# Kernel tuning notes

Measured on AMD Instinct MI355X. Metric: run time of the kernel, lower is better.

## Reference

```python
import jax, jax.numpy as jnp
import numpy as np

D_HEAD = 64
MASK_FILL = -1000000.0


def setup_inputs() -> dict:
    key = jax.random.key(0)
    ks = jax.random.split(key, 5)
    batch, seq, d_model, n_heads, d_head = 4, 2048, 1024, 16, D_HEAD
    # xavier_uniform bound for [d_model, n_heads, d_head]: treated as fan_in=d_model, fan_out=n_heads*d_head
    bound_qkv = float(np.sqrt(6.0 / (d_model + n_heads * d_head)))
    bound_out = float(np.sqrt(6.0 / (d_head + n_heads * d_model)))
    return {
        "resid": jax.random.normal(ks[0], (batch, seq, d_model), dtype=jnp.float32),
        "W_Q": jax.random.uniform(ks[1], (d_model, n_heads, d_head), jnp.float32, -bound_qkv, bound_qkv),
        "W_K": jax.random.uniform(ks[2], (d_model, n_heads, d_head), jnp.float32, -bound_qkv, bound_qkv),
        "W_V": jax.random.uniform(ks[3], (d_model, n_heads, d_head), jnp.float32, -bound_qkv, bound_qkv),
        "W_out": jax.random.uniform(ks[4], (d_head, n_heads, d_model), jnp.float32, -bound_out, bound_out),
        "b_out": jnp.zeros((d_model,), dtype=jnp.float32),
    }


def reference(resid, W_Q, W_K, W_V, W_out, b_out):
    # resid: [b, s, d]; W_Q/K/V: [d, h, dh]; W_out: [dh, h, d]
    seq = resid.shape[1]
    d_head = W_Q.shape[-1]
    q = jnp.einsum('bsd,dhk->bshk', resid, W_Q)
    k = jnp.einsum('bsd,dhk->bshk', resid, W_K)
    v = jnp.einsum('bsd,dhk->bshk', resid, W_V)
    scores = jnp.einsum('bqhk,bkhd->bhqd', q, k.astype(q.dtype)) if False else jnp.einsum('bqhc,bshc->bhqs', q, k)
    scores = scores / jnp.sqrt(jnp.asarray(d_head, dtype=scores.dtype))
    causal_mask = jnp.triu(jnp.ones((seq, seq), dtype=bool), k=1)
    scores = jnp.where(causal_mask, MASK_FILL, scores)
    probs = jax.nn.softmax(scores, axis=-1)  # [b, h, q, s]
    z = jnp.einsum('bhqs,bshc->bqhc', probs, v)
    out = jnp.einsum('bqhc,chd->bqd', z, W_out) + b_out
    return out
```

## Files before the change

kernel.cpp:

```cpp
#include <hip/hip_runtime.h>
#include <hip/hip_bf16.h>


typedef short s16x8 __attribute__((ext_vector_type(8)));
typedef short s16x4 __attribute__((ext_vector_type(4)));
typedef float f32x4 __attribute__((ext_vector_type(4)));

#define MFMA_BF16(A, B, C) __builtin_amdgcn_mfma_f32_16x16x32_bf16((A), (B), (C), 0, 0, 0)

__device__ __forceinline__ short f2bf(float f) {
    __bf16 h = (__bf16)f;
    return __builtin_bit_cast(short, h);
}

__device__ __forceinline__ void gld16(const unsigned short* g, unsigned short* l) {
    __builtin_amdgcn_global_load_lds(
        (const __attribute__((address_space(1))) unsigned int*)g,
        (__attribute__((address_space(3))) unsigned int*)l, 16, 0, 0);
}

__global__ __launch_bounds__(256) void cast_f32_to_bf16(const float* __restrict__ x,
                                                        unsigned short* __restrict__ y,
                                                        int n4) {
    const int i = blockIdx.x * 256 + threadIdx.x;
    if (i >= n4) return;
    const float4 v = ((const float4*)x)[i];
    s16x4 o;
    o[0] = f2bf(v.x); o[1] = f2bf(v.y); o[2] = f2bf(v.z); o[3] = f2bf(v.w);
    *(s16x4*)(y + (size_t)i * 4) = o;
}

__global__ __launch_bounds__(256) void transpose_w_to_bf16(const float* __restrict__ W,
                                                           unsigned short* __restrict__ Wt) {
    __shared__ unsigned short tile[64][66];
    const int n0 = blockIdx.x * 64, k0 = blockIdx.y * 64;
    const int tx = threadIdx.x & 63, ty = threadIdx.x >> 6;
    #pragma unroll
    for (int i = ty; i < 64; i += 4)
        tile[i][tx] = (unsigned short)f2bf(W[(size_t)(k0 + i) * 1024 + n0 + tx]);
    __syncthreads();
    #pragma unroll
    for (int i = ty; i < 64; i += 4)
        Wt[(size_t)(n0 + i) * 1024 + k0 + tx] = tile[tx][i];
}

__global__ __launch_bounds__(256) void transpose_wout_to_bf16(const float* __restrict__ Wout,
                                                              unsigned short* __restrict__ W2t) {
    __shared__ unsigned short tile[64][66];
    const int d0 = blockIdx.x * 64;
    const int h  = blockIdx.y;
    const int tx = threadIdx.x & 63, ty = threadIdx.x >> 6;
    #pragma unroll
    for (int c = ty; c < 64; c += 4)
        tile[c][tx] = (unsigned short)f2bf(Wout[(size_t)(c * 16 + h) * 1024 + d0 + tx]);
    __syncthreads();
    #pragma unroll
    for (int i = ty; i < 64; i += 4)
        W2t[(size_t)(d0 + i) * 1024 + h * 64 + tx] = tile[tx][i];
}

template <int MODE>
__global__ __launch_bounds__(256, 2) void gemm_bt(
    const unsigned short* __restrict__ A,
    const unsigned short* __restrict__ Bt,
    float* __restrict__ Cf, const float* __restrict__ bias,
    unsigned short* __restrict__ Qb, unsigned short* __restrict__ Kb,
    unsigned short* __restrict__ Vt,
    int M, int N, int K)
{
    __shared__ __align__(16) unsigned short As[128 * 32];
    __shared__ __align__(16) unsigned short Bs[128 * 32];
    const int tid  = threadIdx.x;
    const int lane = tid & 63;
    const int w    = tid >> 6;
    const int wm   = w & 1, wn = w >> 1;
    const int quad = lane >> 4, fl = lane & 15;
    const int m0 = blockIdx.y * 128, n0 = blockIdx.x * 128;
    const int lrow = tid >> 2;
    const int lcol = (tid & 3) * 8;

    const unsigned short* Ap = A  + (size_t)(m0 + lrow) * K + lcol;
    const unsigned short* Bp = Bt + (size_t)(n0 + lrow) * K + lcol;

    f32x4 acc[4][4];
    #pragma unroll
    for (int i = 0; i < 4; ++i)
        #pragma unroll
        for (int j = 0; j < 4; ++j)
            acc[i][j] = (f32x4){0.f, 0.f, 0.f, 0.f};

    for (int kt = 0; kt < K; kt += 32) {
        __syncthreads();
        gld16(Ap + kt,                 As + tid * 8);
        gld16(Ap + (size_t)64 * K + kt, As + 2048 + tid * 8);
        gld16(Bp + kt,                 Bs + tid * 8);
        gld16(Bp + (size_t)64 * K + kt, Bs + 2048 + tid * 8);
        __syncthreads();
        s16x8 af[4], bf[4];
        #pragma unroll
        for (int mi = 0; mi < 4; ++mi)
            af[mi] = *(const s16x8*)(As + (wm * 64 + mi * 16 + fl) * 32 + quad * 8);
        #pragma unroll
        for (int ni = 0; ni < 4; ++ni)
            bf[ni] = *(const s16x8*)(Bs + (wn * 64 + ni * 16 + fl) * 32 + quad * 8);
        #pragma unroll
        for (int mi = 0; mi < 4; ++mi)
            #pragma unroll
            for (int ni = 0; ni < 4; ++ni)
                acc[mi][ni] = MFMA_BF16(af[mi], bf[ni], acc[mi][ni]);
    }

    if (MODE == 0) {
        #pragma unroll
        for (int ni = 0; ni < 4; ++ni) {
            const int col = n0 + wn * 64 + ni * 16 + fl;
            const float bv = bias[col];
            #pragma unroll
            for (int mi = 0; mi < 4; ++mi) {
                const int row = m0 + wm * 64 + mi * 16 + quad * 4;
                #pragma unroll
                for (int r = 0; r < 4; ++r)
                    Cf[(size_t)(row + r) * N + col] = acc[mi][ni][r] + bv;
            }
        }
    } else {
        #pragma unroll
        for (int ni = 0; ni < 4; ++ni) {
            const int colg = n0 + wn * 64 + ni * 16 + fl;
            #pragma unroll
            for (int mi = 0; mi < 4; ++mi) {
                const int token = m0 + wm * 64 + mi * 16 + quad * 4;
                if (n0 < 1024) {
                    #pragma unroll
                    for (int r = 0; r < 4; ++r)
                        Qb[(size_t)(token + r) * 1024 + colg] = (unsigned short)f2bf(acc[mi][ni][r]);
                } else if (n0 < 2048) {
                    #pragma unroll
                    for (int r = 0; r < 4; ++r)
                        Kb[(size_t)(token + r) * 1024 + (colg - 1024)] = (unsigned short)f2bf(acc[mi][ni][r]);
                } else {
                    const int cc = colg - 2048;
                    const int hh = cc >> 6, cl = cc & 63;
                    const int bb = token >> 11, ss = token & 2047;
                    s16x4 pv;
                    pv[0] = f2bf(acc[mi][ni][0]); pv[1] = f2bf(acc[mi][ni][1]);
                    pv[2] = f2bf(acc[mi][ni][2]); pv[3] = f2bf(acc[mi][ni][3]);
                    *(s16x4*)(Vt + (size_t)((bb * 16 + hh) * 64 + cl) * 2048 + ss) = pv;
                }
            }
        }
    }
}

__global__ __launch_bounds__(256, 3) void attn_causal(
    const unsigned short* __restrict__ Qb,
    const unsigned short* __restrict__ Kb,
    const unsigned short* __restrict__ Vt,
    unsigned short* __restrict__ Zb)
{
    __shared__ __align__(16) unsigned short KV[17920];
    __shared__ __align__(16) unsigned short Pb[4][32 * 40];
    const int tid = threadIdx.x, lane = tid & 63, w = tid >> 6;
    const int quad = lane >> 4, fl = lane & 15;
    const int lid = blockIdx.x;
    const int qb = 15 - (lid >> 6);
    const int bh = lid & 63, b = bh >> 4, h = bh & 15;
    const int q0 = qb * 128 + w * 32;

    const unsigned short* Kbase = Kb + (size_t)b * 2048 * 1024 + h * 64;
    const unsigned short* Vbase = Vt + (size_t)bh * 64 * 2048;
    unsigned short* PbW = Pb[w];
    const unsigned short* Vs = KV + 9216;

    s16x8 qfr[2][2];
    #pragma unroll
    for (int g = 0; g < 2; ++g) {
        const unsigned short* Qrow = Qb + (size_t)(b * 2048 + q0 + g * 16 + fl) * 1024 + h * 64;
        qfr[g][0] = *(const s16x8*)(Qrow + quad * 8);
        qfr[g][1] = *(const s16x8*)(Qrow + 32 + quad * 8);
    }

    const unsigned short* gsp[9];
    int smul[9];
    unsigned ldsb[9];
    #pragma unroll
    for (int i = 0; i < 9; ++i) {
        const int W = w + 4 * i;
        if (W < 35) {
            const int c = W * 64 + lane;
            if (c < 1152) {
                const int r = c / 9, cl0 = c % 9;
                const int cl = (cl0 == 8) ? 0 : cl0;
                gsp[i] = Kbase + r * 1024 + cl * 8;  smul[i] = 1024;
            } else {
                const int cc = c - 1152;
                const int r = cc / 17, cl0 = cc % 17;
                const int cl = (cl0 == 16) ? 0 : cl0;
                gsp[i] = Vbase + r * 2048 + cl * 8;  smul[i] = 1;
            }
            ldsb[i] = (unsigned)c * 8u;
        }
    }

    f32x4 zt[2][4];
    #pragma unroll
    for (int g = 0; g < 2; ++g)
        #pragma unroll
        for (int mf = 0; mf < 4; ++mf) zt[g][mf] = (f32x4){0.f, 0.f, 0.f, 0.f};
    float ls[2] = {0.f, 0.f};
    const float SC = 0.18033688011112042f;
    const float M  = 32.0f;
    const int ntiles = qb + 1;

    for (int kt = 0; kt < ntiles; ++kt) {
        const int s0 = kt << 7;
        const bool diag = (kt == qb);
        __syncthreads();
        #pragma unroll
        for (int i = 0; i < 9; ++i)
            if (w + 4 * i < 35)
                gld16(gsp[i] + s0 * smul[i], KV + ldsb[i]);
        __syncthreads();

        #pragma unroll
        for (int c4 = 0; c4 < 4; ++c4) {
            if (diag && c4 > w) break;
            #pragma unroll
            for (int e = 0; e < 2; ++e) {
                const int f = 2 * c4 + e;
                const unsigned short* Krow = KV + (f * 16 + fl) * 72;
                const s16x8 kf0 = *(const s16x8*)(Krow + quad * 8);
                const s16x8 kf1 = *(const s16x8*)(Krow + 32 + quad * 8);
                #pragma unroll
                for (int g = 0; g < 2; ++g) {
                    unsigned short* pw = PbW + (g * 16 + fl) * 40 + e * 16 + quad * 4;
                    if (diag && f > 2 * w + g) {
                        *(s16x4*)pw = (s16x4){0, 0, 0, 0};
                    } else {
                        f32x4 z = (f32x4){0.f, 0.f, 0.f, 0.f};
                        z = MFMA_BF16(kf0, qfr[g][0], z);
                        z = MFMA_BF16(kf1, qfr[g][1], z);
                        const bool edge = diag && (f == 2 * w + g);
                        const int qi = q0 + g * 16 + fl;
                        s16x4 pk;
                        #pragma unroll
                        for (int r = 0; r < 4; ++r) {
                            float arg = fmaf(z[r], SC, -M);
                            if (edge) {
                                const int s = s0 + f * 16 + quad * 4 + r;
                                if (s > qi) arg = -1e30f;
                            }
                            const float p = exp2f(arg);
                            ls[g] += p;
                            pk[r] = f2bf(p);
                        }
                        *(s16x4*)pw = pk;
                    }
                }
            }
            const s16x8 pf0 = *(const s16x8*)(PbW + fl * 40 + quad * 8);
            const s16x8 pf1 = *(const s16x8*)(PbW + (16 + fl) * 40 + quad * 8);
            #pragma unroll
            for (int mf = 0; mf < 4; ++mf) {
                const s16x8 vf = *(const s16x8*)(
                    Vs + (mf * 16 + fl) * 136 + c4 * 32 + quad * 8);
                zt[0][mf] = MFMA_BF16(vf, pf0, zt[0][mf]);
                zt[1][mf] = MFMA_BF16(vf, pf1, zt[1][mf]);
            }
        }
    }
    #pragma unroll
    for (int g = 0; g < 2; ++g) {
        float lt = ls[g];
        lt += __shfl_xor(lt, 16);
        lt += __shfl_xor(lt, 32);
        const float inv = 1.0f / lt;
        unsigned short* Zrow = Zb + (size_t)(b * 2048 + q0 + g * 16 + fl) * 1024 + h * 64;
        #pragma unroll
        for (int mf = 0; mf < 4; ++mf) {
            s16x4 o;
            o[0] = f2bf(zt[g][mf][0] * inv); o[1] = f2bf(zt[g][mf][1] * inv);
            o[2] = f2bf(zt[g][mf][2] * inv); o[3] = f2bf(zt[g][mf][3] * inv);
            *(s16x4*)(Zrow + mf * 16 + quad * 4) = o;
        }
    }
}

extern "C" void kernel_launch(void* const* d_in, const int* in_sizes, int n_in,
                              void* d_out, int out_size, void* d_ws, size_t ws_size,
                              hipStream_t stream) {
    const float* resid = (const float*)d_in[0];
    const float* WQ    = (const float*)d_in[1];
    const float* WK    = (const float*)d_in[2];
    const float* WV    = (const float*)d_in[3];
    const float* Wout  = (const float*)d_in[4];
    const float* bout  = (const float*)d_in[5];
    float* out = (float*)d_out;

    char* p = (char*)d_ws;
    auto alloc = [&](size_t bytes) { void* r = (void*)p; p += (bytes + 255) & ~(size_t)255; return r; };
    unsigned short* residb = (unsigned short*)alloc(8192ull * 1024 * 2);
    unsigned short* Wqkvt  = (unsigned short*)alloc(3072ull * 1024 * 2);
    unsigned short* W2t    = (unsigned short*)alloc(1024ull * 1024 * 2);
    unsigned short* Qbuf   = (unsigned short*)alloc(8192ull * 1024 * 2);
    unsigned short* Kbuf   = (unsigned short*)alloc(8192ull * 1024 * 2);
    unsigned short* Vtb    = (unsigned short*)alloc(64ull * 64 * 2048 * 2);
    unsigned short* Zbuf   = (unsigned short*)alloc(8192ull * 1024 * 2);

    cast_f32_to_bf16<<<8192, 256, 0, stream>>>(resid, residb, 2097152);
    transpose_w_to_bf16<<<dim3(16, 16), 256, 0, stream>>>(WQ, Wqkvt);
    transpose_w_to_bf16<<<dim3(16, 16), 256, 0, stream>>>(WK, Wqkvt + 1024 * 1024);
    transpose_w_to_bf16<<<dim3(16, 16), 256, 0, stream>>>(WV, Wqkvt + 2 * 1024 * 1024);
    transpose_wout_to_bf16<<<dim3(16, 16), 256, 0, stream>>>(Wout, W2t);

    gemm_bt<1><<<dim3(24, 64), 256, 0, stream>>>(residb, Wqkvt, nullptr, nullptr,
                                                 Qbuf, Kbuf, Vtb, 8192, 3072, 1024);
    attn_causal<<<1024, 256, 0, stream>>>(Qbuf, Kbuf, Vtb, Zbuf);
    gemm_bt<0><<<dim3(8, 64), 256, 0, stream>>>(Zbuf, W2t, out, bout,
                                                nullptr, nullptr, nullptr, 8192, 1024, 1024);
}
```

Measured before the change: 281.5 us.

## Fuse prep kernels, deepen GEMM K-tile, and share KV tiles across 8-wave attention blocks

The five preprocessing launches (resid cast plus weight transposes) become a single kernel that dispatches on block index. The GEMM loads a 64-wide K slice per iteration into a padded shared buffer, using 9 global-to-LDS loads per thread, which halves the number of barrier pairs. Attention blocks grow to 512 threads covering 256 queries, so each KV tile load is shared by eight waves. The lower-half waves skip tiles beyond their diagonal, which costs some idle time and changes occupancy.

```diff
diff --git a/kernel.cpp b/kernel.cpp
--- a/kernel.cpp
+++ b/kernel.cpp
@@ -19,44 +19,48 @@
         (__attribute__((address_space(3))) unsigned int*)l, 16, 0, 0);
 }
 
-__global__ __launch_bounds__(256) void cast_f32_to_bf16(const float* __restrict__ x,
-                                                        unsigned short* __restrict__ y,
-                                                        int n4) {
-    const int i = blockIdx.x * 256 + threadIdx.x;
-    if (i >= n4) return;
-    const float4 v = ((const float4*)x)[i];
-    s16x4 o;
-    o[0] = f2bf(v.x); o[1] = f2bf(v.y); o[2] = f2bf(v.z); o[3] = f2bf(v.w);
-    *(s16x4*)(y + (size_t)i * 4) = o;
-}
-
-__global__ __launch_bounds__(256) void transpose_w_to_bf16(const float* __restrict__ W,
-                                                           unsigned short* __restrict__ Wt) {
+__global__ __launch_bounds__(256) void prep_fused(
+    const float* __restrict__ resid, const float* __restrict__ WQ,
+    const float* __restrict__ WK, const float* __restrict__ WV,
+    const float* __restrict__ Wout,
+    unsigned short* __restrict__ residb, unsigned short* __restrict__ Wqkvt,
+    unsigned short* __restrict__ W2t)
+{
+    const int bid = blockIdx.x;
+    if (bid < 8192) {
+        const int i = bid * 256 + threadIdx.x;
+        const float4 v = ((const float4*)resid)[i];
+        s16x4 o;
+        o[0] = f2bf(v.x); o[1] = f2bf(v.y); o[2] = f2bf(v.z); o[3] = f2bf(v.w);
+        *(s16x4*)(residb + (size_t)i * 4) = o;
+        return;
+    }
     __shared__ unsigned short tile[64][66];
-    const int n0 = blockIdx.x * 64, k0 = blockIdx.y * 64;
+    const int id2 = bid - 8192;
+    const int which = id2 >> 8;
+    const int sub = id2 & 255;
     const int tx = threadIdx.x & 63, ty = threadIdx.x >> 6;
-    #pragma unroll
-    for (int i = ty; i < 64; i += 4)
-        tile[i][tx] = (unsigned short)f2bf(W[(size_t)(k0 + i) * 1024 + n0 + tx]);
-    __syncthreads();
-    #pragma unroll
-    for (int i = ty; i < 64; i += 4)
-        Wt[(size_t)(n0 + i) * 1024 + k0 + tx] = tile[tx][i];
-}
-
-__global__ __launch_bounds__(256) void transpose_wout_to_bf16(const float* __restrict__ Wout,
-                                                              unsigned short* __restrict__ W2t) {
-    __shared__ unsigned short tile[64][66];
-    const int d0 = blockIdx.x * 64;
-    const int h  = blockIdx.y;
-    const int tx = threadIdx.x & 63, ty = threadIdx.x >> 6;
-    #pragma unroll
-    for (int c = ty; c < 64; c += 4)
-        tile[c][tx] = (unsigned short)f2bf(Wout[(size_t)(c * 16 + h) * 1024 + d0 + tx]);
-    __syncthreads();
-    #pragma unroll
-    for (int i = ty; i < 64; i += 4)
-        W2t[(size_t)(d0 + i) * 1024 + h * 64 + tx] = tile[tx][i];
+    if (which < 3) {
+        const float* W = which == 0 ? WQ : (which == 1 ? WK : WV);
+        unsigned short* Wt = Wqkvt + (size_t)which * 1024 * 1024;
+        const int n0 = (sub & 15) * 64, k0 = (sub >> 4) * 64;
+        #pragma unroll
+        for (int i = ty; i < 64; i += 4)
+            tile[i][tx] = (unsigned short)f2bf(W[(size_t)(k0 + i) * 1024 + n0 + tx]);
+        __syncthreads();
+        #pragma unroll
+        for (int i = ty; i < 64; i += 4)
+            Wt[(size_t)(n0 + i) * 1024 + k0 + tx] = tile[tx][i];
+    } else {
+        const int d0 = (sub & 15) * 64, h = sub >> 4;
+        #pragma unroll
+        for (int c = ty; c < 64; c += 4)
+            tile[c][tx] = (unsigned short)f2bf(Wout[(size_t)(c * 16 + h) * 1024 + d0 + tx]);
+        __syncthreads();
+        #pragma unroll
+        for (int i = ty; i < 64; i += 4)
+            W2t[(size_t)(d0 + i) * 1024 + h * 64 + tx] = tile[tx][i];
+    }
 }
 
 template <int MODE>
@@ -68,19 +72,25 @@
     unsigned short* __restrict__ Vt,
     int M, int N, int K)
 {
-    __shared__ __align__(16) unsigned short As[128 * 32];
-    __shared__ __align__(16) unsigned short Bs[128 * 32];
+    __shared__ __align__(16) unsigned short AB[2 * 128 * 72];
     const int tid  = threadIdx.x;
     const int lane = tid & 63;
     const int w    = tid >> 6;
     const int wm   = w & 1, wn = w >> 1;
     const int quad = lane >> 4, fl = lane & 15;
     const int m0 = blockIdx.y * 128, n0 = blockIdx.x * 128;
-    const int lrow = tid >> 2;
-    const int lcol = (tid & 3) * 8;
-
-    const unsigned short* Ap = A  + (size_t)(m0 + lrow) * K + lcol;
-    const unsigned short* Bp = Bt + (size_t)(n0 + lrow) * K + lcol;
+
+    const unsigned short* gp[9];
+    unsigned ldso[9];
+    #pragma unroll
+    for (int i = 0; i < 9; ++i) {
+        const int c = i * 256 + tid;
+        const int cm = c % 1152;
+        const int r = cm / 9, cl0 = cm % 9;
+        const int cl = (cl0 == 8) ? 0 : cl0;
+        gp[i] = (c < 1152 ? A + (size_t)(m0 + r) * K : Bt + (size_t)(n0 + r) * K) + cl * 8;
+        ldso[i] = (unsigned)c * 8u;
+    }
 
     f32x4 acc[4][4];
     #pragma unroll
@@ -89,25 +99,27 @@
         for (int j = 0; j < 4; ++j)
             acc[i][j] = (f32x4){0.f, 0.f, 0.f, 0.f};
 
-    for (int kt = 0; kt < K; kt += 32) {
-        __syncthreads();
-        gld16(Ap + kt,                 As + tid * 8);
-        gld16(Ap + (size_t)64 * K + kt, As + 2048 + tid * 8);
-        gld16(Bp + kt,                 Bs + tid * 8);
-        gld16(Bp + (size_t)64 * K + kt, Bs + 2048 + tid * 8);
-        __syncthreads();
-        s16x8 af[4], bf[4];
-        #pragma unroll
-        for (int mi = 0; mi < 4; ++mi)
-            af[mi] = *(const s16x8*)(As + (wm * 64 + mi * 16 + fl) * 32 + quad * 8);
-        #pragma unroll
-        for (int ni = 0; ni < 4; ++ni)
-            bf[ni] = *(const s16x8*)(Bs + (wn * 64 + ni * 16 + fl) * 32 + quad * 8);
-        #pragma unroll
-        for (int mi = 0; mi < 4; ++mi)
+    for (int kt = 0; kt < K; kt += 64) {
+        __syncthreads();
+        #pragma unroll
+        for (int i = 0; i < 9; ++i)
+            gld16(gp[i] + kt, AB + ldso[i]);
+        __syncthreads();
+        #pragma unroll
+        for (int ko = 0; ko < 2; ++ko) {
+            s16x8 af[4], bf[4];
+            #pragma unroll
+            for (int mi = 0; mi < 4; ++mi)
+                af[mi] = *(const s16x8*)(AB + (wm * 64 + mi * 16 + fl) * 72 + ko * 32 + quad * 8);
             #pragma unroll
             for (int ni = 0; ni < 4; ++ni)
-                acc[mi][ni] = MFMA_BF16(af[mi], bf[ni], acc[mi][ni]);
+                bf[ni] = *(const s16x8*)(AB + 9216 + (wn * 64 + ni * 16 + fl) * 72 + ko * 32 + quad * 8);
+            #pragma unroll
+            for (int mi = 0; mi < 4; ++mi)
+                #pragma unroll
+                for (int ni = 0; ni < 4; ++ni)
+                    acc[mi][ni] = MFMA_BF16(af[mi], bf[ni], acc[mi][ni]);
+        }
     }
 
     if (MODE == 0) {
@@ -152,20 +164,23 @@
     }
 }
 
-__global__ __launch_bounds__(256, 3) void attn_causal(
+__global__ __launch_bounds__(512, 4) void attn_causal(
     const unsigned short* __restrict__ Qb,
     const unsigned short* __restrict__ Kb,
     const unsigned short* __restrict__ Vt,
     unsigned short* __restrict__ Zb)
 {
     __shared__ __align__(16) unsigned short KV[17920];
-    __shared__ __align__(16) unsigned short Pb[4][32 * 40];
+    __shared__ __align__(16) unsigned short Pb[8][32 * 40];
     const int tid = threadIdx.x, lane = tid & 63, w = tid >> 6;
     const int quad = lane >> 4, fl = lane & 15;
     const int lid = blockIdx.x;
-    const int qb = 15 - (lid >> 6);
+    const int g8 = lid >> 6;
+    const int qb = g8 < 4 ? 7 - g8 : g8 - 4;
     const int bh = lid & 63, b = bh >> 4, h = bh & 15;
-    const int q0 = qb * 128 + w * 32;
+    const int wq0 = qb * 256 + w * 32;
+    const int wl = w & 3;
+    const int dt = 2 * qb + (w >> 2);
 
     const unsigned short* Kbase = Kb + (size_t)b * 2048 * 1024 + h * 64;
     const unsigned short* Vbase = Vt + (size_t)bh * 64 * 2048;
@@ -175,17 +190,17 @@
     s16x8 qfr[2][2];
     #pragma unroll
     for (int g = 0; g < 2; ++g) {
-        const unsigned short* Qrow = Qb + (size_t)(b * 2048 + q0 + g * 16 + fl) * 1024 + h * 64;
+        const unsigned short* Qrow = Qb + (size_t)(b * 2048 + wq0 + g * 16 + fl) * 1024 + h * 64;
         qfr[g][0] = *(const s16x8*)(Qrow + quad * 8);
         qfr[g][1] = *(const s16x8*)(Qrow + 32 + quad * 8);
     }
 
-    const unsigned short* gsp[9];
-    int smul[9];
-    unsigned ldsb[9];
-    #pragma unroll
-    for (int i = 0; i < 9; ++i) {
-        const int W = w + 4 * i;
+    const unsigned short* gsp[5];
+    int smul[5];
+    unsigned ldsb[5];
+    #pragma unroll
+    for (int i = 0; i < 5; ++i) {
+        const int W = w + 8 * i;
         if (W < 35) {
             const int c = W * 64 + lane;
             if (c < 1152) {
@@ -210,21 +225,22 @@
     float ls[2] = {0.f, 0.f};
     const float SC = 0.18033688011112042f;
     const float M  = 32.0f;
-    const int ntiles = qb + 1;
+    const int ntiles = 2 * qb + 2;
 
     for (int kt = 0; kt < ntiles; ++kt) {
         const int s0 = kt << 7;
-        const bool diag = (kt == qb);
-        __syncthreads();
-        #pragma unroll
-        for (int i = 0; i < 9; ++i)
-            if (w + 4 * i < 35)
+        __syncthreads();
+        #pragma unroll
+        for (int i = 0; i < 5; ++i)
+            if (w + 8 * i < 35)
                 gld16(gsp[i] + s0 * smul[i], KV + ldsb[i]);
         __syncthreads();
 
+        if (kt > dt) continue;
+        const bool diag = (kt == dt);
         #pragma unroll
         for (int c4 = 0; c4 < 4; ++c4) {
-            if (diag && c4 > w) break;
+            if (diag && c4 > wl) break;
             #pragma unroll
             for (int e = 0; e < 2; ++e) {
                 const int f = 2 * c4 + e;
@@ -234,14 +250,14 @@
                 #pragma unroll
                 for (int g = 0; g < 2; ++g) {
                     unsigned short* pw = PbW + (g * 16 + fl) * 40 + e * 16 + quad * 4;
-                    if (diag && f > 2 * w + g) {
+                    if (diag && f > 2 * wl + g) {
                         *(s16x4*)pw = (s16x4){0, 0, 0, 0};
                     } else {
                         f32x4 z = (f32x4){0.f, 0.f, 0.f, 0.f};
                         z = MFMA_BF16(kf0, qfr[g][0], z);
                         z = MFMA_BF16(kf1, qfr[g][1], z);
-                        const bool edge = diag && (f == 2 * w + g);
-                        const int qi = q0 + g * 16 + fl;
+                        const bool edge = diag && (f == 2 * wl + g);
+                        const int qi = wq0 + g * 16 + fl;
                         s16x4 pk;
                         #pragma unroll
                         for (int r = 0; r < 4; ++r) {
@@ -275,7 +291,7 @@
         lt += __shfl_xor(lt, 16);
         lt += __shfl_xor(lt, 32);
         const float inv = 1.0f / lt;
-        unsigned short* Zrow = Zb + (size_t)(b * 2048 + q0 + g * 16 + fl) * 1024 + h * 64;
+        unsigned short* Zrow = Zb + (size_t)(b * 2048 + wq0 + g * 16 + fl) * 1024 + h * 64;
         #pragma unroll
         for (int mf = 0; mf < 4; ++mf) {
             s16x4 o;
@@ -307,15 +323,10 @@
     unsigned short* Vtb    = (unsigned short*)alloc(64ull * 64 * 2048 * 2);
     unsigned short* Zbuf   = (unsigned short*)alloc(8192ull * 1024 * 2);
 
-    cast_f32_to_bf16<<<8192, 256, 0, stream>>>(resid, residb, 2097152);
-    transpose_w_to_bf16<<<dim3(16, 16), 256, 0, stream>>>(WQ, Wqkvt);
-    transpose_w_to_bf16<<<dim3(16, 16), 256, 0, stream>>>(WK, Wqkvt + 1024 * 1024);
-    transpose_w_to_bf16<<<dim3(16, 16), 256, 0, stream>>>(WV, Wqkvt + 2 * 1024 * 1024);
-    transpose_wout_to_bf16<<<dim3(16, 16), 256, 0, stream>>>(Wout, W2t);
-
+    prep_fused<<<9216, 256, 0, stream>>>(resid, WQ, WK, WV, Wout, residb, Wqkvt, W2t);
     gemm_bt<1><<<dim3(24, 64), 256, 0, stream>>>(residb, Wqkvt, nullptr, nullptr,
                                                  Qbuf, Kbuf, Vtb, 8192, 3072, 1024);
-    attn_causal<<<1024, 256, 0, stream>>>(Qbuf, Kbuf, Vtb, Zbuf);
+    attn_causal<<<512, 512, 0, stream>>>(Qbuf, Kbuf, Vtb, Zbuf);
     gemm_bt<0><<<dim3(8, 64), 256, 0, stream>>>(Zbuf, W2t, out, bout,
                                                 nullptr, nullptr, nullptr, 8192, 1024, 1024);
 }
```

New measurement: 258.5 us. 1.09x faster.
